# Kernel tuning notes

Measured on AMD Instinct MI355X. Metric: run time of the kernel, lower is better.

The kernel has to match this reference:

```python
import jax, jax.numpy as jnp
import numpy as np

CHUNK = 64

def depthwise_fir(x, filt):
    # x: [B,N,H,D]; filt: [H,D,K]; causal depthwise FIR conv along N
    B, N, H, D = x.shape
    K = filt.shape[-1]
    xc = x.reshape(B, N, H * D).transpose(0, 2, 1)  # [B, HD, N]
    xc = jnp.pad(xc, ((0, 0), (0, 0), (K - 1, 0)))
    w = filt.reshape(H * D, 1, K)
    y = jax.lax.conv_general_dilated(xc, w, (1,), 'VALID',
                                     feature_group_count=H * D,
                                     dimension_numbers=('NCH', 'OIH', 'NCH'))
    return y.transpose(0, 2, 1).reshape(B, N, H, D)

def delta_rule_chunkwise(q, k, v, beta, chunk=CHUNK):
    # DeltaNet chunkwise parallel delta rule. q,k,v:[B,H,L,D], beta:[B,H,L]
    B, H, L, D = q.shape
    q = q * (D ** -0.5)
    k = k / (jnp.linalg.norm(k, axis=-1, keepdims=True) + 1e-6)  # l2-norm keys (DeltaNet convention)
    v = v * beta[..., None]
    k_beta = k * beta[..., None]
    n = L // chunk
    toc = lambda t: t.reshape(B, H, n, chunk, D)
    qc, kc, vc, kbc = toc(q), toc(k), toc(v), toc(k_beta)
    # T = (I + strict_lower(k_beta k^T))^{-1} via triangular solve
    A = jnp.tril(jnp.einsum('bhncd,bhnmd->bhncm', kbc, kc), -1)
    I = jnp.eye(chunk, dtype=q.dtype)
    T = jax.scipy.linalg.solve_triangular(I + A, jnp.broadcast_to(I, A.shape), lower=True)
    u = T @ vc   # [B,H,n,c,D]
    w = T @ kbc  # [B,H,n,c,D]
    def step(S, inp):
        q_i, k_i, u_i, w_i = inp                 # [B,H,c,D]
        u_t = u_i - w_i @ S
        attn_i = jnp.tril(jnp.einsum('bhcd,bhmd->bhcm', q_i, k_i))
        o_i = q_i @ S + attn_i @ u_t
        S = S + jnp.einsum('bhcd,bhce->bhde', k_i, u_t)
        return S, o_i
    xs = tuple(jnp.moveaxis(t, 2, 0) for t in (qc, kc, u, w))
    S0 = jnp.zeros((B, H, D, D), dtype=q.dtype)
    S, o = jax.lax.scan(step, S0, xs)
    o = jnp.moveaxis(o, 0, 2).reshape(B, H, L, D)
    return o, S

def setup_inputs() -> dict:
    key = jax.random.key(0)
    B, N, C, H = 4, 1024, 768, 12
    D = C // H
    P = 5
    ks = jax.random.split(key, 16)
    s = 0.02
    fir_s = jnp.zeros((H, D, 3)).at[..., -1].set(1.0) + 0.01 * jax.random.normal(ks[1], (H, D, 3))
    fir_l = jnp.zeros((H, D, 7)).at[..., -1].set(1.0) + 0.01 * jax.random.normal(ks[2], (H, D, 7))
    return {
        'x': jax.random.normal(ks[0], (B, N, C), jnp.float32),
        'w_qkv': s * jax.random.normal(ks[3], (C, 3 * C)),
        'w_proj': s * jax.random.normal(ks[4], (C, C)),
        'b_proj': jnp.zeros((C,)),
        'fir_short_w': fir_s,
        'fir_long_w': fir_l,
        'mix': 0.02 * jax.random.normal(ks[5], (H, H)),
        'w_prune': s * jax.random.normal(ks[6], (C, H * P)),
        'b_prune': jnp.zeros((H * P,)),
        'w_g1': s * jax.random.normal(ks[7], (C, C)),
        'b_g1': jnp.zeros((C,)),
        'w_g2': s * jax.random.normal(ks[8], (C, H)),
        'b_g2': jnp.zeros((H,)),
        'w_id': s * jax.random.normal(ks[9], (C, C)),
        'id_static_logit': jnp.full((H,), float(np.log(0.2 / 0.8)), jnp.float32),
        'w_idgate': s * jax.random.normal(ks[10], (C, H)),
        'b_idgate': jnp.full((H,), -1.5, jnp.float32),
    }

def reference(x, w_qkv, w_proj, b_proj, fir_short_w, fir_long_w, mix, w_prune,
              b_prune, w_g1, b_g1, w_g2, b_g2, w_id, id_static_logit, w_idgate, b_idgate):
    B, N, C = x.shape
    H = id_static_logit.shape[0]
    D = C // H
    qkv = (x @ w_qkv).reshape(B, N, 3, H, D).transpose(2, 0, 3, 1, 4)  # [3,B,H,N,D]
    q, k, v = qkv[0], qkv[1], qkv[2]
    scale = D ** -0.5
    scores = jnp.einsum('bhqd,bhkd->bhqk', q, k) * scale
    # causal softmax attention (fp8 sage-attention math in full precision)
    neg = jnp.finfo(scores.dtype).min
    causal = jnp.tril(jnp.ones((N, N), dtype=bool))
    attn = jax.nn.softmax(jnp.where(causal, scores, neg), axis=-1)
    attn_out = jnp.einsum('bhqk,bhkd->bnhd'.replace('n', 'q'), attn, v).transpose(0, 2, 1, 3)  # [B,N,H,D] (unused downstream, kept for fidelity)
    v_reshaped = v.transpose(0, 2, 1, 3)  # [B,N,H,D]
    # identity path with static*dynamic gate
    identity_out = (x @ w_id).reshape(B, N, H, D)
    dyn_gate = jax.nn.sigmoid(x @ w_idgate + b_idgate)   # [B,N,H]
    static_gate = jax.nn.sigmoid(id_static_logit)
    identity_out = identity_out * (dyn_gate * static_gate)[..., None]
    # beta = row-sums of (non-causal) softmax, per source (== ~1 numerically)
    beta = jax.nn.softmax(scores, axis=-1).sum(-1)       # [B,H,N]
    delta_out = delta_rule_chunkwise(q, k, v, beta)[0].transpose(0, 2, 1, 3)  # [B,N,H,D]
    # FIR paths + cross-head mixing (residual head-mixing matrix)
    fir_s = depthwise_fir(v_reshaped, fir_short_w)
    fir_l = depthwise_fir(v_reshaped, fir_long_w)
    mix_s = fir_s + jnp.einsum('bnhd,hg->bngd', fir_s, mix)
    mix_l = fir_l + jnp.einsum('bnhd,hg->bngd', fir_l, mix)
    paths = jnp.stack([mix_s, mix_l, delta_out, v_reshaped, identity_out], 0)  # [P,B,N,H,D]
    P = paths.shape[0]
    # progressive pruning: per-head softmax over paths + entropy loss
    wts = jax.nn.softmax((x @ w_prune + b_prune).reshape(B, N, H, P), axis=-1)
    pruned = jnp.einsum('pbnhd,bnhp->bnhd', paths, wts)
    ent1 = -jnp.mean(jnp.sum(wts * jnp.log(wts + 1e-8), -1))
    # context gating: MLP -> per-head sigmoid gate + binary entropy loss
    hdn = jax.nn.gelu(x @ w_g1 + b_g1)
    gate = jax.nn.sigmoid(hdn @ w_g2 + b_g2)             # [B,N,H]
    context = pruned * gate[..., None]
    ent2 = -jnp.mean(gate * jnp.log(gate + 1e-8) + (1 - gate) * jnp.log(1 - gate + 1e-8))
    out = context.reshape(B, N, C) @ w_proj + b_proj
    return out, ent1 + ent2
```

## Files before the change

### kernel.cpp

```cpp
#include <hip/hip_runtime.h>
#include <hip/hip_bf16.h>
#include <math.h>

#define Bz 4
#define Nn 1024
#define Cc 768
#define Hh 12
#define Dd 64
#define BN 4096
#define NC 16
#define BH 48
#define OUT_ELEMS 3145728

#define WS_U       0u
#define WS_PLIG    3145728u
#define WS_GL      3670016u
#define WS_ENT     4194304u
#define WS_FIRST   4195328u
#define WS_FIRLT   4197632u
#define WS_CBIAS   4203008u
#define WS_GBIAS   4206976u
#define WS_SH      4207104u
#define SH_XB      0u
#define SH_QKVB    3145728u
#define SH_IDOUT   12582912u
#define SH_HDNB    15728640u
#define SH_CTXB    18874368u
#define SH_DELTA   22020096u
#define SH_QS      25165824u
#define SH_KNT     28311552u
#define SH_W       31457280u
#define SH_AT      34603008u
#define SH_WCAT2T  37748736u
#define SH_G2T     40796160u
#define SH_WPROJT  40894464u

typedef __attribute__((ext_vector_type(8))) short bf16x8;
typedef __attribute__((ext_vector_type(4))) float f32x4;

__device__ __forceinline__ float sigmoidf_(float x) { return 1.f / (1.f + __expf(-x)); }
__device__ __forceinline__ float geluf_(float x) {
    float t = tanhf(0.7978845608028654f * (x + 0.044715f * x * x * x));
    return 0.5f * x * (1.f + t);
}
__device__ __forceinline__ short bf16c(float f) {
    union { float f; unsigned u; } a; a.f = f;
    unsigned r = a.u + 0x7fffu + ((a.u >> 16) & 1u);
    return (short)(r >> 16);
}
__device__ __forceinline__ float b2f(short s) {
    union { float f; unsigned u; } a;
    a.u = ((unsigned)(unsigned short)s) << 16;
    return a.f;
}
__device__ __forceinline__ void gload16(const void* g, void* l) {
    __builtin_amdgcn_global_load_lds(
        (const __attribute__((address_space(1))) unsigned*)g,
        (__attribute__((address_space(3))) unsigned*)l, 16, 0, 0);
}
__device__ __forceinline__ bf16x8 frag_(const short* arr, int row, int kc, int quad) {
    return *(const bf16x8*)&arr[row * 64 + (((kc * 4 + quad) ^ (row & 7)) << 3)];
}

__global__ __launch_bounds__(256) void convert_x_kernel(const float* __restrict__ src,
        short* __restrict__ dst, int n4) {
    int i = blockIdx.x * 256 + threadIdx.x;
    if (i < n4) {
        float4 v = *(const float4*)&src[(size_t)i * 4];
        short4 o;
        o.x = bf16c(v.x); o.y = bf16c(v.y); o.z = bf16c(v.z); o.w = bf16c(v.w);
        *(short4*)&dst[(size_t)i * 4] = o;
    }
}

__global__ __launch_bounds__(256) void convert_w_kernel(const float* __restrict__ w_qkv,
        const float* __restrict__ w_id, const float* __restrict__ w_g1,
        const float* __restrict__ w_proj, short* __restrict__ wcat2T,
        short* __restrict__ wprojT,
        const float* __restrict__ wp, const float* __restrict__ wig,
        const float* __restrict__ bp, const float* __restrict__ big,
        const float* __restrict__ bg1, const float* __restrict__ bg2,
        const float* __restrict__ wg2, const float* __restrict__ firs,
        const float* __restrict__ firl, short* __restrict__ g2T,
        float* __restrict__ cbias, float* __restrict__ gbias,
        float* __restrict__ firsT, float* __restrict__ firlT) {
    __shared__ float t[64][65];
    const int z = blockIdx.z;
    const int tid = threadIdx.x;
    if (z == 4) {
        int i = (blockIdx.y * 12 + blockIdx.x) * 256 + tid;
        if (i < 98304) {
            int r = i / 768, k = i % 768;
            float wv = 0.f;
            if (r < 60) wv = wp[k * 60 + r];
            else if (r < 72) wv = wig[k * 12 + (r - 60)];
            wcat2T[(size_t)(3840 + r) * 768 + k] = (r < 72) ? bf16c(wv) : (short)0;
            g2T[(size_t)r * 768 + k] = (r < 12) ? bf16c(wg2[k * 12 + r]) : (short)0;
        }
        if (i < 3968) {
            float bv = 0.f;
            if (i >= 3072 && i < 3840) bv = bg1[i - 3072];
            else if (i >= 3840 && i < 3900) bv = bp[i - 3840];
            else if (i >= 3900 && i < 3912) bv = big[i - 3900];
            cbias[i] = bv;
        }
        if (i < 128) gbias[i] = (i < 12) ? bg2[i] : 0.f;
        if (i < 2304) { int tt = i / 768, e = i % 768; firsT[tt * 768 + e] = firs[e * 3 + tt]; }
        if (i < 5376) { int tt = i / 768, e = i % 768; firlT[tt * 768 + e] = firl[e * 7 + tt]; }
        return;
    }
    const float* src; short* dst; int Nw;
    if (z == 0)      { src = w_qkv;  dst = wcat2T;               Nw = 2304; }
    else if (z == 1) { src = w_id;   dst = wcat2T + 2304 * 768;  Nw = 768; }
    else if (z == 2) { src = w_g1;   dst = wcat2T + 3072 * 768;  Nw = 768; }
    else             { src = w_proj; dst = wprojT;               Nw = 768; }
    const int n0 = blockIdx.y * 64;
    if (n0 >= Nw) return;
    const int k0 = blockIdx.x * 64;
    for (int e = tid; e < 1024; e += 256) {
        int r = e >> 4, c4 = (e & 15) * 4;
        float4 v = *(const float4*)&src[(size_t)(k0 + r) * Nw + n0 + c4];
        t[c4 + 0][r] = v.x; t[c4 + 1][r] = v.y;
        t[c4 + 2][r] = v.z; t[c4 + 3][r] = v.w;
    }
    __syncthreads();
    for (int e = tid; e < 1024; e += 256) {
        int r = e >> 4, c4 = (e & 15) * 4;
        short4 o;
        o.x = bf16c(t[r][c4 + 0]); o.y = bf16c(t[r][c4 + 1]);
        o.z = bf16c(t[r][c4 + 2]); o.w = bf16c(t[r][c4 + 3]);
        *(short4*)&dst[(size_t)(n0 + r) * 768 + k0 + c4] = o;
    }
}

#define GEMM_CORE(APTR, BPTR, KDIM)                                            \
    __shared__ short As[128 * 64];                                             \
    __shared__ short Bs[128 * 64];                                             \
    const int tid = threadIdx.x;                                               \
    const int lane = tid & 63, w = tid >> 6;                                   \
    const int quad = lane >> 4, l15 = lane & 15;                               \
    const int L_ = blockIdx.y * gridDim.x + blockIdx.x;                        \
    const int xcd_ = L_ & 7, j_ = L_ >> 3;                                     \
    const int row0 = (xcd_ * 4 + (j_ & 3)) * 128, col0 = (j_ >> 2) * 128;      \
    const int wm = (w >> 1) * 64, wn = (w & 1) * 64;                           \
    int srow[4]; int scol[4];                                                  \
    _Pragma("unroll") for (int i = 0; i < 4; ++i) {                            \
        int G = (w * 4 + i) * 64 + lane;                                       \
        int row = G >> 3, g = G & 7;                                           \
        srow[i] = row;                                                         \
        scol[i] = (g ^ (row & 7)) * 8;                                         \
    }                                                                          \
    int aoff[4][2], boff[4][2];                                                \
    _Pragma("unroll") for (int mi = 0; mi < 4; ++mi)                           \
        _Pragma("unroll") for (int kk = 0; kk < 2; ++kk) {                     \
            int ra = wm + mi * 16 + l15;                                       \
            aoff[mi][kk] = ra * 128 + (((kk * 4 + quad) ^ (ra & 7)) * 16);     \
            int rb = wn + mi * 16 + l15;                                       \
            boff[mi][kk] = rb * 128 + (((kk * 4 + quad) ^ (rb & 7)) * 16);     \
        }                                                                      \
    f32x4 acc[4][4];                                                           \
    _Pragma("unroll") for (int mi = 0; mi < 4; ++mi)                           \
        _Pragma("unroll") for (int ni = 0; ni < 4; ++ni) acc[mi][ni] = (f32x4)0.f; \
    for (int k0 = 0; k0 < (KDIM); k0 += 64) {                                  \
        _Pragma("unroll") for (int i = 0; i < 4; ++i) {                        \
            gload16(&(APTR)[(size_t)(row0 + srow[i]) * (KDIM) + k0 + scol[i]], \
                    &As[(w * 4 + i) * 512]);                                   \
            gload16(&(BPTR)[(size_t)(col0 + srow[i]) * (KDIM) + k0 + scol[i]], \
                    &Bs[(w * 4 + i) * 512]);                                   \
        }                                                                      \
        __syncthreads();                                                       \
        _Pragma("unroll") for (int kk = 0; kk < 2; ++kk) {                     \
            bf16x8 af[4], bfr[4];                                              \
            _Pragma("unroll") for (int mi = 0; mi < 4; ++mi)                   \
                af[mi] = *(const bf16x8*)((const char*)As + aoff[mi][kk]);     \
            _Pragma("unroll") for (int ni = 0; ni < 4; ++ni)                   \
                bfr[ni] = *(const bf16x8*)((const char*)Bs + boff[ni][kk]);    \
            _Pragma("unroll") for (int mi = 0; mi < 4; ++mi)                   \
                _Pragma("unroll") for (int ni = 0; ni < 4; ++ni)               \
                    acc[mi][ni] = __builtin_amdgcn_mfma_f32_16x16x32_bf16(     \
                        af[mi], bfr[ni], acc[mi][ni], 0, 0, 0);                \
        }                                                                      \
        __syncthreads();                                                       \
    }

__global__ __launch_bounds__(256) void gemm_main(const short* __restrict__ A,
        const short* __restrict__ BT, const float* __restrict__ bias,
        short* __restrict__ qkvb, short* __restrict__ idoutb,
        short* __restrict__ hdnb, float* __restrict__ plig) {
    GEMM_CORE(A, BT, 768)
#pragma unroll
    for (int ni = 0; ni < 4; ++ni) {
        int col = col0 + wn + ni * 16 + l15;
        float bv = bias[col];
#pragma unroll
        for (int mi = 0; mi < 4; ++mi) {
#pragma unroll
            for (int r = 0; r < 4; ++r) {
                int row = row0 + wm + mi * 16 + quad * 4 + r;
                float v = acc[mi][ni][r] + bv;
                if (col < 2304) {
                    qkvb[(size_t)row * 2304 + col] = bf16c(v);
                } else if (col < 3072) {
                    idoutb[(size_t)row * 768 + (col - 2304)] = bf16c(v);
                } else if (col < 3840) {
                    hdnb[(size_t)row * 768 + (col - 3072)] = bf16c(geluf_(v));
                } else {
                    plig[(size_t)row * 128 + (col - 3840)] = v;
                }
            }
        }
    }
}

__global__ __launch_bounds__(256) void gemm_mfma(const short* __restrict__ A,
        const short* __restrict__ BT, const float* __restrict__ bias,
        float* __restrict__ C, int M, int N, int K) {
    GEMM_CORE(A, BT, K)
#pragma unroll
    for (int ni = 0; ni < 4; ++ni) {
        int col = col0 + wn + ni * 16 + l15;
        float bv = bias ? bias[col] : 0.f;
#pragma unroll
        for (int mi = 0; mi < 4; ++mi) {
#pragma unroll
            for (int r = 0; r < 4; ++r) {
                int row = row0 + wm + mi * 16 + quad * 4 + r;
                C[(size_t)row * N + col] = acc[mi][ni][r] + bv;
            }
        }
    }
}

__global__ __launch_bounds__(256) void pre_kernel(const short* __restrict__ qkvb,
        short* __restrict__ Qsb16, short* __restrict__ Kntb16, float* __restrict__ U,
        short* __restrict__ Wb16, short* __restrict__ Atb16) {
    __shared__ __align__(16) char smem[50176];
    float (*ts)[68] = (float (*)[68])smem;
    short* kn  = (short*)(smem + 17408);
    short* knt = (short*)(smem + 25600);
    short* qsb = (short*)(smem + 33792);
    short* vtb = (short*)(smem + 41984);
    float (*zbuf)[68] = (float (*)[68])(smem + 17408);
    short* tb  = (short*)(smem + 33792);
    const int blk = blockIdx.x;
    const int c = blk & 15, bh = blk >> 4;
    const int b = bh / Hh, h = bh % Hh;
    const int tid = threadIdx.x;
    const int lane = tid & 63, w = tid >> 6;
    const int quad = lane >> 4, l15 = lane & 15;
    const int r = tid >> 2, d0 = (tid & 3) * 16;
    const size_t rowb = ((size_t)(b * Nn + c * 64)) * 2304 + h * 64;
    const size_t base2 = (size_t)blk * 4096;

    {
        const short* qp = &qkvb[rowb + (size_t)r * 2304 + d0];
        bf16x8 qb0 = *(const bf16x8*)&qp[0],    qb1 = *(const bf16x8*)&qp[8];
        bf16x8 kb0 = *(const bf16x8*)&qp[768],  kb1 = *(const bf16x8*)&qp[776];
        bf16x8 vb0 = *(const bf16x8*)&qp[1536], vb1 = *(const bf16x8*)&qp[1544];

        float kf[16];
#pragma unroll
        for (int t = 0; t < 8; ++t) { kf[t] = b2f(kb0[t]); kf[8 + t] = b2f(kb1[t]); }
        float ss = 0.f;
#pragma unroll
        for (int t = 0; t < 16; ++t) ss += kf[t] * kf[t];
        ss += __shfl_xor(ss, 1);
        ss += __shfl_xor(ss, 2);
        float invn = 1.f / (sqrtf(ss) + 1e-6f);
        {
            bf16x8 g0, g1;
#pragma unroll
            for (int t = 0; t < 8; ++t) {
                g0[t] = bf16c(kf[t] * invn); g1[t] = bf16c(kf[8 + t] * invn);
            }
            int gb = d0 >> 3;
            *(bf16x8*)&kn[r * 64 + (((gb + 0) ^ (r & 7)) << 3)] = g0;
            *(bf16x8*)&kn[r * 64 + (((gb + 1) ^ (r & 7)) << 3)] = g1;
#pragma unroll
            for (int t = 0; t < 8; ++t) {
                int d = d0 + t;
                knt[d * 64 + (((r >> 3) ^ (d & 7)) << 3) + (r & 7)] = g0[t];
                int d2 = d0 + 8 + t;
                knt[d2 * 64 + (((r >> 3) ^ (d2 & 7)) << 3) + (r & 7)] = g1[t];
            }
        }
        {
            bf16x8 g0, g1;
#pragma unroll
            for (int t = 0; t < 8; ++t) {
                g0[t] = bf16c(b2f(qb0[t]) * 0.125f);
                g1[t] = bf16c(b2f(qb1[t]) * 0.125f);
            }
            int gb = d0 >> 3;
            *(bf16x8*)&qsb[r * 64 + (((gb + 0) ^ (r & 7)) << 3)] = g0;
            *(bf16x8*)&qsb[r * 64 + (((gb + 1) ^ (r & 7)) << 3)] = g1;
            *(bf16x8*)&Qsb16[base2 + r * 64 + d0] = g0;
            *(bf16x8*)&Qsb16[base2 + r * 64 + d0 + 8] = g1;
        }
#pragma unroll
        for (int t = 0; t < 8; ++t) {
            int d = d0 + t;
            vtb[d * 64 + (((r >> 3) ^ (d & 7)) << 3) + (r & 7)] = vb0[t];
            int d2 = d0 + 8 + t;
            vtb[d2 * 64 + (((r >> 3) ^ (d2 & 7)) << 3) + (r & 7)] = vb1[t];
        }
    }
    __syncthreads();

    f32x4 accT[4];
    {
        const int ar = w * 16 + l15;
        bf16x8 aK0 = frag_(kn, ar, 0, quad), aK1 = frag_(kn, ar, 1, quad);
        bf16x8 aQ0 = frag_(qsb, ar, 0, quad), aQ1 = frag_(qsb, ar, 1, quad);
        f32x4 accA[4];
#pragma unroll
        for (int ni = 0; ni < 4; ++ni) {
            int br = ni * 16 + l15;
            bf16x8 b0 = frag_(kn, br, 0, quad), b1 = frag_(kn, br, 1, quad);
            accA[ni] = __builtin_amdgcn_mfma_f32_16x16x32_bf16(aK0, b0, (f32x4)0.f, 0, 0, 0);
            accA[ni] = __builtin_amdgcn_mfma_f32_16x16x32_bf16(aK1, b1, accA[ni], 0, 0, 0);
            accT[ni] = __builtin_amdgcn_mfma_f32_16x16x32_bf16(aQ0, b0, (f32x4)0.f, 0, 0, 0);
            accT[ni] = __builtin_amdgcn_mfma_f32_16x16x32_bf16(aQ1, b1, accT[ni], 0, 0, 0);
        }
#pragma unroll
        for (int ni = 0; ni < 4; ++ni)
#pragma unroll
            for (int reg = 0; reg < 4; ++reg) {
                int row = w * 16 + quad * 4 + reg;
                int col = ni * 16 + l15;
                ts[row][col] = (col < row) ? accA[ni][reg] : 0.f;
            }
    }
    __syncthreads();

    {
        const int R0 = w * 16;
        const int j = lane & 15, s = lane >> 4;
#pragma unroll 1
        for (int i = 0; i < 16; ++i) {
            float p = 0.f;
            for (int m = s; m < i; m += 4)
                p += ts[R0 + i][R0 + m] * ts[R0 + m][R0 + j];
            p += __shfl_xor(p, 16);
            p += __shfl_xor(p, 32);
            if (s == 0) ts[R0 + i][R0 + j] = ((j == i) ? 1.f : 0.f) - p;
        }
    }
    __syncthreads();
#pragma unroll 1
    for (int I = 1; I < 4; ++I) {
        const int ncol = I * 16;
        for (int e = tid; e < 16 * ncol; e += 256) {
            int i = e / ncol, jj = e % ncol;
            float s = 0.f;
            for (int m = jj; m < ncol; ++m) s += ts[ncol + i][m] * ts[m][jj];
            zbuf[i][jj] = s;
        }
        __syncthreads();
        for (int e = tid; e < 16 * ncol; e += 256) {
            int i = e / ncol, jj = e % ncol;
            float s = 0.f;
            for (int ml = 0; ml <= i; ++ml) s += ts[ncol + i][ncol + ml] * zbuf[ml][jj];
            ts[ncol + i][jj] = -s;
        }
        __syncthreads();
    }
    for (int e = tid; e < 512; e += 256) {
        int row = e >> 3, g = e & 7;
        bf16x8 o;
#pragma unroll
        for (int t = 0; t < 8; ++t) o[t] = bf16c(ts[row][g * 8 + t]);
        *(bf16x8*)&tb[row * 64 + ((g ^ (row & 7)) << 3)] = o;
    }
    __syncthreads();

    f32x4 accW[4], accU[4];
    {
        const int ar = w * 16 + l15;
        bf16x8 aT0 = frag_(tb, ar, 0, quad), aT1 = frag_(tb, ar, 1, quad);
#pragma unroll
        for (int ni = 0; ni < 4; ++ni) {
            int br = ni * 16 + l15;
            bf16x8 b0 = frag_(knt, br, 0, quad), b1 = frag_(knt, br, 1, quad);
            bf16x8 c0 = frag_(vtb, br, 0, quad), c1 = frag_(vtb, br, 1, quad);
            accW[ni] = __builtin_amdgcn_mfma_f32_16x16x32_bf16(aT0, b0, (f32x4)0.f, 0, 0, 0);
            accW[ni] = __builtin_amdgcn_mfma_f32_16x16x32_bf16(aT1, b1, accW[ni], 0, 0, 0);
            accU[ni] = __builtin_amdgcn_mfma_f32_16x16x32_bf16(aT0, c0, (f32x4)0.f, 0, 0, 0);
            accU[ni] = __builtin_amdgcn_mfma_f32_16x16x32_bf16(aT1, c1, accU[ni], 0, 0, 0);
        }
    }
#pragma unroll
    for (int ni = 0; ni < 4; ++ni)
#pragma unroll
        for (int reg = 0; reg < 4; ++reg) {
            int row = w * 16 + quad * 4 + reg;
            int col = ni * 16 + l15;
            Wb16[base2 + (size_t)row * 64 + col] = bf16c(accW[ni][reg]);
            U[base2 + (size_t)row * 64 + col] = accU[ni][reg];
            Atb16[base2 + (size_t)row * 64 + col] =
                (col <= row) ? bf16c(accT[ni][reg]) : (short)0;
        }
    for (int e = tid; e < 512; e += 256) {
        int row = e >> 3, gl = e & 7;
        *(bf16x8*)&Kntb16[base2 + row * 64 + ((gl ^ (row & 7)) << 3)] =
            *(const bf16x8*)&knt[row * 64 + (gl << 3)];
    }
}

#define LOADF(cc, F, UU) {                                                     \
    size_t tb_ = ((size_t)(bh * 16 + (cc))) * 4096;                            \
    F##0 = *(const bf16x8*)&Wb16[tb_ + off0];                                  \
    F##1 = *(const bf16x8*)&Wb16[tb_ + off1];                                  \
    F##2 = *(const bf16x8*)&Qsb16[tb_ + off0];                                 \
    F##3 = *(const bf16x8*)&Qsb16[tb_ + off1];                                 \
    F##4 = *(const bf16x8*)&Atb16[tb_ + off0];                                 \
    F##5 = *(const bf16x8*)&Atb16[tb_ + off1];                                 \
    F##6 = *(const bf16x8*)&Kntb16[tb_ + off0];                                \
    F##7 = *(const bf16x8*)&Kntb16[tb_ + off1];                                \
    UU##0 = U[tb_ + urow + 0 * 64]; UU##1 = U[tb_ + urow + 1 * 64];            \
    UU##2 = U[tb_ + urow + 2 * 64]; UU##3 = U[tb_ + urow + 3 * 64]; }

#define BODY(c, F, UU, FN, UN) {                                               \
    int cn_ = ((c) + 1 < 16) ? (c) + 1 : 0;                                    \
    LOADF(cn_, FN, UN);                                                        \
    bf16x8 st0 = *(const bf16x8*)&ST[stoff0];                                  \
    bf16x8 st1 = *(const bf16x8*)&ST[stoff1];                                  \
    bf16x8 nw0, nw1;                                                           \
    _Pragma("unroll") for (int t_ = 0; t_ < 8; ++t_) {                         \
        nw0[t_] = F##0[t_] ^ (short)0x8000;                                    \
        nw1[t_] = F##1[t_] ^ (short)0x8000; }                                  \
    f32x4 ut = {UU##0, UU##1, UU##2, UU##3};                                   \
    ut = __builtin_amdgcn_mfma_f32_16x16x32_bf16(nw0, st0, ut, 0, 0, 0);       \
    ut = __builtin_amdgcn_mfma_f32_16x16x32_bf16(nw1, st1, ut, 0, 0, 0);       \
    f32x4 o = (f32x4)0.f;                                                      \
    o = __builtin_amdgcn_mfma_f32_16x16x32_bf16(F##2, st0, o, 0, 0, 0);        \
    o = __builtin_amdgcn_mfma_f32_16x16x32_bf16(F##3, st1, o, 0, 0, 0);        \
    _Pragma("unroll") for (int j_ = 0; j_ < 4; ++j_) {                         \
        int rr_ = R0 + quad * 4 + j_;                                          \
        UT[l15 * 64 + (((rr_ >> 3) ^ (l15 & 7)) << 3) + (rr_ & 7)] = bf16c(ut[j_]); } \
    __syncthreads();                                                           \
    bf16x8 uf0 = *(const bf16x8*)&UT[stoff0];                                  \
    bf16x8 uf1 = *(const bf16x8*)&UT[stoff1];                                  \
    o = __builtin_amdgcn_mfma_f32_16x16x32_bf16(F##4, uf0, o, 0, 0, 0);        \
    o = __builtin_amdgcn_mfma_f32_16x16x32_bf16(F##5, uf1, o, 0, 0, 0);        \
    S = __builtin_amdgcn_mfma_f32_16x16x32_bf16(F##6, uf0, S, 0, 0, 0);        \
    S = __builtin_amdgcn_mfma_f32_16x16x32_bf16(F##7, uf1, S, 0, 0, 0);        \
    _Pragma("unroll") for (int j_ = 0; j_ < 4; ++j_)                           \
        deltab[obase + (size_t)((c) * 64 + j_) * 768] = bf16c(o[j_]);          \
    _Pragma("unroll") for (int j_ = 0; j_ < 4; ++j_) {                         \
        int dd_ = R0 + quad * 4 + j_;                                          \
        ST[l15 * 64 + (((dd_ >> 3) ^ (l15 & 7)) << 3) + (dd_ & 7)] = bf16c(S[j_]); } \
    __syncthreads(); }

__global__ __launch_bounds__(256) void scan_kernel(const short* __restrict__ Qsb16,
        const short* __restrict__ Kntb16, const float* __restrict__ U,
        const short* __restrict__ Wb16, const short* __restrict__ Atb16,
        short* __restrict__ deltab) {
    __shared__ short ST[1024];
    __shared__ short UT[1024];
    const int bh = blockIdx.x;
    const int b = bh / Hh, h = bh % Hh;
    const int g0 = blockIdx.y * 16;
    const int tid = threadIdx.x;
    const int lane = tid & 63, w = tid >> 6;
    const int quad = lane >> 4, l15 = lane & 15;
    const int R0 = w * 16;
    const int off0 = (R0 + l15) * 64 + quad * 8;
    const int off1 = off0 + 32;
    const int urow = (R0 + quad * 4) * 64 + g0 + l15;
    const int stoff0 = l15 * 64 + ((quad ^ (l15 & 7)) << 3);
    const int stoff1 = l15 * 64 + (((4 + quad) ^ (l15 & 7)) << 3);
    const size_t obase = ((size_t)(b * Nn + R0 + quad * 4)) * 768 + h * 64 + g0 + l15;

    for (int e = tid; e < 512; e += 256) ((int*)ST)[e] = 0;
    f32x4 S = (f32x4)0.f;
    bf16x8 fA0, fA1, fA2, fA3, fA4, fA5, fA6, fA7;
    bf16x8 fB0, fB1, fB2, fB3, fB4, fB5, fB6, fB7;
    float uA0, uA1, uA2, uA3, uB0, uB1, uB2, uB3;
    LOADF(0, fA, uA);
    __syncthreads();
#pragma unroll 1
    for (int c = 0; c < 16; c += 2) {
        BODY(c, fA, uA, fB, uB);
        BODY(c + 1, fB, uB, fA, uA);
    }
}

__global__ __launch_bounds__(256) void paths_kernel(const short* __restrict__ qkvb,
        const short* __restrict__ deltab, const short* __restrict__ idoutb,
        const float* __restrict__ plig, const float* __restrict__ gl,
        const float* __restrict__ mixw, const float* __restrict__ idst,
        const float* __restrict__ firsT, const float* __restrict__ firlT,
        short* __restrict__ ctxb, float* __restrict__ entslots) {
    __shared__ float vt[10][768];
    __shared__ float fsb[768], flb[768];
    __shared__ float wts4[4][60], gate4[4][12], idg4[4][12];
    __shared__ float entb[48];
    const int blk = blockIdx.x;
    const int b = blk >> 8, n0 = (blk & 255) * 4;
    const int tid = threadIdx.x;

    for (int t = tid; t < 960; t += 256) {
        int row = t / 96, c8 = (t % 96) * 8;
        int np = n0 - 6 + row;
        float4 lo = make_float4(0.f, 0.f, 0.f, 0.f);
        float4 hi = make_float4(0.f, 0.f, 0.f, 0.f);
        if (np >= 0) {
            bf16x8 vv = *(const bf16x8*)&qkvb[((size_t)((b << 10) + np)) * 2304 + 1536 + c8];
            lo.x = b2f(vv[0]); lo.y = b2f(vv[1]); lo.z = b2f(vv[2]); lo.w = b2f(vv[3]);
            hi.x = b2f(vv[4]); hi.y = b2f(vv[5]); hi.z = b2f(vv[6]); hi.w = b2f(vv[7]);
        }
        *(float4*)&vt[row][c8] = lo;
        *(float4*)&vt[row][c8 + 4] = hi;
    }
    if (tid < 48) {
        int ni = tid / 12, h = tid % 12;
        int bn = (b << 10) + n0 + ni;
        const float* pb = &plig[(size_t)bn * 128];
        float lg[5]; float mx = -1e30f;
#pragma unroll
        for (int p = 0; p < 5; ++p) { lg[p] = pb[h * 5 + p]; mx = fmaxf(mx, lg[p]); }
        float sum = 0.f;
#pragma unroll
        for (int p = 0; p < 5; ++p) { lg[p] = __expf(lg[p] - mx); sum += lg[p]; }
        float e1 = 0.f;
#pragma unroll
        for (int p = 0; p < 5; ++p) {
            float wv = lg[p] / sum;
            wts4[ni][h * 5 + p] = wv;
            e1 += wv * logf(wv + 1e-8f);
        }
        float g = sigmoidf_(gl[(size_t)bn * 128 + h]);
        gate4[ni][h] = g;
        float e2 = g * logf(g + 1e-8f) + (1.f - g) * logf(1.f - g + 1e-8f);
        idg4[ni][h] = sigmoidf_(pb[60 + h]) * sigmoidf_(idst[h]);
        entb[tid] = e1 + e2;
    }
    float4 wl[7], wsv[3];
    if (tid < 192) {
        int c4 = tid * 4;
#pragma unroll
        for (int t = 0; t < 7; ++t) wl[t] = *(const float4*)&firlT[t * 768 + c4];
#pragma unroll
        for (int t = 0; t < 3; ++t) wsv[t] = *(const float4*)&firsT[t * 768 + c4];
    }
    __syncthreads();

#pragma unroll 1
    for (int ni = 0; ni < 4; ++ni) {
        if (tid < 192) {
            int c4 = tid * 4;
            float4 as = make_float4(0.f, 0.f, 0.f, 0.f);
            float4 al = make_float4(0.f, 0.f, 0.f, 0.f);
#pragma unroll
            for (int t = 0; t < 7; ++t) {
                float4 vv = *(const float4*)&vt[ni + t][c4];
                al.x += wl[t].x * vv.x; al.y += wl[t].y * vv.y;
                al.z += wl[t].z * vv.z; al.w += wl[t].w * vv.w;
                if (t >= 4) {
                    as.x += wsv[t - 4].x * vv.x; as.y += wsv[t - 4].y * vv.y;
                    as.z += wsv[t - 4].z * vv.z; as.w += wsv[t - 4].w * vv.w;
                }
            }
            *(float4*)&fsb[c4] = as;
            *(float4*)&flb[c4] = al;
        }
        __syncthreads();
        if (tid < 192) {
            int c4 = tid * 4;
            int h = c4 >> 6, d = c4 & 63;
            float4 ms = *(const float4*)&fsb[c4];
            float4 ml = *(const float4*)&flb[c4];
#pragma unroll
            for (int hh = 0; hh < 12; ++hh) {
                float mw = mixw[hh * 12 + h];
                float4 fsv = *(const float4*)&fsb[hh * 64 + d];
                float4 flv = *(const float4*)&flb[hh * 64 + d];
                ms.x += mw * fsv.x; ms.y += mw * fsv.y;
                ms.z += mw * fsv.z; ms.w += mw * fsv.w;
                ml.x += mw * flv.x; ml.y += mw * flv.y;
                ml.z += mw * flv.z; ml.w += mw * flv.w;
            }
            int bn = (b << 10) + n0 + ni;
            short4 ds = *(const short4*)&deltab[(size_t)bn * 768 + c4];
            short4 is = *(const short4*)&idoutb[(size_t)bn * 768 + c4];
            float4 vv = *(const float4*)&vt[ni + 6][c4];
            float ig = idg4[ni][h];
            const float* wp = &wts4[ni][h * 5];
            float4 pr;
            pr.x = ms.x * wp[0] + ml.x * wp[1] + b2f(ds.x) * wp[2] + vv.x * wp[3] + b2f(is.x) * ig * wp[4];
            pr.y = ms.y * wp[0] + ml.y * wp[1] + b2f(ds.y) * wp[2] + vv.y * wp[3] + b2f(is.y) * ig * wp[4];
            pr.z = ms.z * wp[0] + ml.z * wp[1] + b2f(ds.z) * wp[2] + vv.z * wp[3] + b2f(is.z) * ig * wp[4];
            pr.w = ms.w * wp[0] + ml.w * wp[1] + b2f(ds.w) * wp[2] + vv.w * wp[3] + b2f(is.w) * ig * wp[4];
            float g = gate4[ni][h];
            short4 o;
            o.x = bf16c(pr.x * g); o.y = bf16c(pr.y * g);
            o.z = bf16c(pr.z * g); o.w = bf16c(pr.w * g);
            *(short4*)&ctxb[(size_t)bn * 768 + c4] = o;
        }
        __syncthreads();
    }
    if (tid == 0) {
        float s = 0.f;
#pragma unroll
        for (int i = 0; i < 48; ++i) s += entb[i];
        entslots[blk] = s;
    }
}

__global__ __launch_bounds__(256) void finalize_kernel(const float* __restrict__ slots,
        float* __restrict__ out) {
    __shared__ float red[256];
    const int tid = threadIdx.x;
    float s = 0.f;
    for (int i = tid; i < 1024; i += 256) s += slots[i];
    red[tid] = s;
    __syncthreads();
    for (int off = 128; off > 0; off >>= 1) {
        if (tid < off) red[tid] += red[tid + off];
        __syncthreads();
    }
    if (tid == 0) out[OUT_ELEMS] = -red[0] * (1.f / 49152.f);
}

extern "C" void kernel_launch(void* const* d_in, const int* in_sizes, int n_in,
                              void* d_out, int out_size, void* d_ws, size_t ws_size,
                              hipStream_t stream) {
    const float* x        = (const float*)d_in[0];
    const float* w_qkv    = (const float*)d_in[1];
    const float* w_proj   = (const float*)d_in[2];
    const float* b_proj   = (const float*)d_in[3];
    const float* fir_s_w  = (const float*)d_in[4];
    const float* fir_l_w  = (const float*)d_in[5];
    const float* mixw     = (const float*)d_in[6];
    const float* w_prune  = (const float*)d_in[7];
    const float* b_prune  = (const float*)d_in[8];
    const float* w_g1     = (const float*)d_in[9];
    const float* b_g1     = (const float*)d_in[10];
    const float* w_g2     = (const float*)d_in[11];
    const float* b_g2     = (const float*)d_in[12];
    const float* w_id     = (const float*)d_in[13];
    const float* id_st    = (const float*)d_in[14];
    const float* w_idgate = (const float*)d_in[15];
    const float* b_idgate = (const float*)d_in[16];
    float* out = (float*)d_out;
    float* ws  = (float*)d_ws;

    float* Ub    = ws + WS_U;
    float* plig  = ws + WS_PLIG;
    float* gl    = ws + WS_GL;
    float* ent   = ws + WS_ENT;
    float* firsT = ws + WS_FIRST;
    float* firlT = ws + WS_FIRLT;
    float* cbias = ws + WS_CBIAS;
    float* gbias = ws + WS_GBIAS;
    short* wsh   = (short*)(ws + WS_SH);
    short* xb      = wsh + SH_XB;
    short* qkvb    = wsh + SH_QKVB;
    short* idoutb  = wsh + SH_IDOUT;
    short* hdnb    = wsh + SH_HDNB;
    short* ctxb    = wsh + SH_CTXB;
    short* deltab  = wsh + SH_DELTA;
    short* Qsb16   = wsh + SH_QS;
    short* Kntb16  = wsh + SH_KNT;
    short* Wb16    = wsh + SH_W;
    short* Atb16   = wsh + SH_AT;
    short* wcat2T  = wsh + SH_WCAT2T;
    short* g2T     = wsh + SH_G2T;
    short* wprojT  = wsh + SH_WPROJT;

    convert_x_kernel<<<dim3(3072), 256, 0, stream>>>(x, xb, 786432);
    convert_w_kernel<<<dim3(12, 36, 5), 256, 0, stream>>>(w_qkv, w_id, w_g1, w_proj,
            wcat2T, wprojT, w_prune, w_idgate, b_prune, b_idgate, b_g1, b_g2,
            w_g2, fir_s_w, fir_l_w, g2T, cbias, gbias, firsT, firlT);
    gemm_main<<<dim3(31, 32), 256, 0, stream>>>(xb, wcat2T, cbias,
                                                qkvb, idoutb, hdnb, plig);
    gemm_mfma<<<dim3(1, 32), 256, 0, stream>>>(hdnb, g2T, gbias, gl, BN, 128, 768);
    pre_kernel<<<dim3(BH * NC), 256, 0, stream>>>(qkvb, Qsb16, Kntb16, Ub, Wb16, Atb16);
    scan_kernel<<<dim3(BH, 4), 256, 0, stream>>>(Qsb16, Kntb16, Ub, Wb16, Atb16, deltab);
    paths_kernel<<<dim3(1024), 256, 0, stream>>>(qkvb, deltab, idoutb, plig, gl,
                                                 mixw, id_st, firsT, firlT, ctxb, ent);
    gemm_mfma<<<dim3(6, 32), 256, 0, stream>>>(ctxb, wprojT, b_proj, out, BN, 768, 768);
    finalize_kernel<<<1, 256, 0, stream>>>(ent, out);
}
```

Before: 258.2 us.

## Merge small kernels to cut launch count: fold x-convert, gate GEMM, finalize

Folds the x fp32->bf16 conversion into the weight-conversion kernel as an extra z-slice, runs the small gate GEMM (hdn @ w_g2) as 32 extra blocks inside the delta-rule preprocessing kernel, and moves the entropy finalize reduction into the last projection GEMM. This drops three kernel launches and the serialization gaps between them. In exchange, one GEMM block does the serial reduction, and the gate GEMM blocks share a launch with the heavier preprocessing blocks, which can unbalance that launch.

```diff
diff --git a/kernel.cpp b/kernel.cpp
--- a/kernel.cpp
+++ b/kernel.cpp
@@ -62,17 +62,6 @@
     return *(const bf16x8*)&arr[row * 64 + (((kc * 4 + quad) ^ (row & 7)) << 3)];
 }
 
-__global__ __launch_bounds__(256) void convert_x_kernel(const float* __restrict__ src,
-        short* __restrict__ dst, int n4) {
-    int i = blockIdx.x * 256 + threadIdx.x;
-    if (i < n4) {
-        float4 v = *(const float4*)&src[(size_t)i * 4];
-        short4 o;
-        o.x = bf16c(v.x); o.y = bf16c(v.y); o.z = bf16c(v.z); o.w = bf16c(v.w);
-        *(short4*)&dst[(size_t)i * 4] = o;
-    }
-}
-
 __global__ __launch_bounds__(256) void convert_w_kernel(const float* __restrict__ w_qkv,
         const float* __restrict__ w_id, const float* __restrict__ w_g1,
         const float* __restrict__ w_proj, short* __restrict__ wcat2T,
@@ -83,10 +72,21 @@
         const float* __restrict__ wg2, const float* __restrict__ firs,
         const float* __restrict__ firl, short* __restrict__ g2T,
         float* __restrict__ cbias, float* __restrict__ gbias,
-        float* __restrict__ firsT, float* __restrict__ firlT) {
+        float* __restrict__ firsT, float* __restrict__ firlT,
+        const float* __restrict__ x, short* __restrict__ xb) {
     __shared__ float t[64][65];
     const int z = blockIdx.z;
     const int tid = threadIdx.x;
+    if (z == 5) {
+        for (int i = (blockIdx.y * 12 + blockIdx.x) * 256 + tid; i < 786432;
+             i += 110592) {
+            float4 v = *(const float4*)&x[(size_t)i * 4];
+            short4 o;
+            o.x = bf16c(v.x); o.y = bf16c(v.y); o.z = bf16c(v.z); o.w = bf16c(v.w);
+            *(short4*)&xb[(size_t)i * 4] = o;
+        }
+        return;
+    }
     if (z == 4) {
         int i = (blockIdx.y * 12 + blockIdx.x) * 256 + tid;
         if (i < 98304) {
@@ -214,7 +214,9 @@
 
 __global__ __launch_bounds__(256) void gemm_mfma(const short* __restrict__ A,
         const short* __restrict__ BT, const float* __restrict__ bias,
-        float* __restrict__ C, int M, int N, int K) {
+        float* __restrict__ C, int M, int N, int K,
+        const float* __restrict__ slots, float* __restrict__ entout) {
+    __shared__ float red[256];
     GEMM_CORE(A, BT, K)
 #pragma unroll
     for (int ni = 0; ni < 4; ++ni) {
@@ -229,12 +231,100 @@
             }
         }
     }
-}
-
-__global__ __launch_bounds__(256) void pre_kernel(const short* __restrict__ qkvb,
+    if (slots && L_ == 0) {
+        float s = 0.f;
+        for (int i = tid; i < 1024; i += 256) s += slots[i];
+        red[tid] = s;
+        __syncthreads();
+        for (int off = 128; off > 0; off >>= 1) {
+            if (tid < off) red[tid] += red[tid + off];
+            __syncthreads();
+        }
+        if (tid == 0) entout[0] = -red[0] * (1.f / 49152.f);
+    }
+}
+
+__global__ __launch_bounds__(256) void pre_gl_kernel(const short* __restrict__ qkvb,
         short* __restrict__ Qsb16, short* __restrict__ Kntb16, float* __restrict__ U,
-        short* __restrict__ Wb16, short* __restrict__ Atb16) {
+        short* __restrict__ Wb16, short* __restrict__ Atb16,
+        const short* __restrict__ hdnb, const short* __restrict__ g2T,
+        const float* __restrict__ gbias, float* __restrict__ gl) {
     __shared__ __align__(16) char smem[50176];
+    const int blk = blockIdx.x;
+    const int tid = threadIdx.x;
+    const int lane = tid & 63, w = tid >> 6;
+    const int quad = lane >> 4, l15 = lane & 15;
+
+    if (blk >= 768) {
+        short* As = (short*)smem;
+        short* Bs = (short*)(smem + 16384);
+        const int row0 = (blk - 768) * 128;
+        const int wm = (w >> 1) * 64, wn = (w & 1) * 64;
+        int srow[4], scol[4];
+#pragma unroll
+        for (int i = 0; i < 4; ++i) {
+            int G = (w * 4 + i) * 64 + lane;
+            int row = G >> 3, g = G & 7;
+            srow[i] = row;
+            scol[i] = (g ^ (row & 7)) * 8;
+        }
+        int aoff[4][2], boff[4][2];
+#pragma unroll
+        for (int mi = 0; mi < 4; ++mi)
+#pragma unroll
+            for (int kk = 0; kk < 2; ++kk) {
+                int ra = wm + mi * 16 + l15;
+                aoff[mi][kk] = ra * 128 + (((kk * 4 + quad) ^ (ra & 7)) * 16);
+                int rb = wn + mi * 16 + l15;
+                boff[mi][kk] = rb * 128 + (((kk * 4 + quad) ^ (rb & 7)) * 16);
+            }
+        f32x4 acc[4][4];
+#pragma unroll
+        for (int mi = 0; mi < 4; ++mi)
+#pragma unroll
+            for (int ni = 0; ni < 4; ++ni) acc[mi][ni] = (f32x4)0.f;
+        for (int k0 = 0; k0 < 768; k0 += 64) {
+#pragma unroll
+            for (int i = 0; i < 4; ++i) {
+                gload16(&hdnb[(size_t)(row0 + srow[i]) * 768 + k0 + scol[i]],
+                        &As[(w * 4 + i) * 512]);
+                gload16(&g2T[(size_t)srow[i] * 768 + k0 + scol[i]],
+                        &Bs[(w * 4 + i) * 512]);
+            }
+            __syncthreads();
+#pragma unroll
+            for (int kk = 0; kk < 2; ++kk) {
+                bf16x8 af[4], bfr[4];
+#pragma unroll
+                for (int mi = 0; mi < 4; ++mi)
+                    af[mi] = *(const bf16x8*)((const char*)As + aoff[mi][kk]);
+#pragma unroll
+                for (int ni = 0; ni < 4; ++ni)
+                    bfr[ni] = *(const bf16x8*)((const char*)Bs + boff[ni][kk]);
+#pragma unroll
+                for (int mi = 0; mi < 4; ++mi)
+#pragma unroll
+                    for (int ni = 0; ni < 4; ++ni)
+                        acc[mi][ni] = __builtin_amdgcn_mfma_f32_16x16x32_bf16(
+                            af[mi], bfr[ni], acc[mi][ni], 0, 0, 0);
+            }
+            __syncthreads();
+        }
+#pragma unroll
+        for (int ni = 0; ni < 4; ++ni) {
+            int col = wn + ni * 16 + l15;
+            float bv = gbias[col];
+#pragma unroll
+            for (int mi = 0; mi < 4; ++mi)
+#pragma unroll
+                for (int r = 0; r < 4; ++r) {
+                    int row = row0 + wm + mi * 16 + quad * 4 + r;
+                    gl[(size_t)row * 128 + col] = acc[mi][ni][r] + bv;
+                }
+        }
+        return;
+    }
+
     float (*ts)[68] = (float (*)[68])smem;
     short* kn  = (short*)(smem + 17408);
     short* knt = (short*)(smem + 25600);
@@ -242,12 +332,8 @@
     short* vtb = (short*)(smem + 41984);
     float (*zbuf)[68] = (float (*)[68])(smem + 17408);
     short* tb  = (short*)(smem + 33792);
-    const int blk = blockIdx.x;
     const int c = blk & 15, bh = blk >> 4;
     const int b = bh / Hh, h = bh % Hh;
-    const int tid = threadIdx.x;
-    const int lane = tid & 63, w = tid >> 6;
-    const int quad = lane >> 4, l15 = lane & 15;
     const int r = tid >> 2, d0 = (tid & 3) * 16;
     const size_t rowb = ((size_t)(b * Nn + c * 64)) * 2304 + h * 64;
     const size_t base2 = (size_t)blk * 4096;
@@ -401,9 +487,9 @@
                 (col <= row) ? bf16c(accT[ni][reg]) : (short)0;
         }
     for (int e = tid; e < 512; e += 256) {
-        int row = e >> 3, gl = e & 7;
-        *(bf16x8*)&Kntb16[base2 + row * 64 + ((gl ^ (row & 7)) << 3)] =
-            *(const bf16x8*)&knt[row * 64 + (gl << 3)];
+        int row = e >> 3, gl2 = e & 7;
+        *(bf16x8*)&Kntb16[base2 + row * 64 + ((gl2 ^ (row & 7)) << 3)] =
+            *(const bf16x8*)&knt[row * 64 + (gl2 << 3)];
     }
 }
 
@@ -608,21 +694,6 @@
     }
 }
 
-__global__ __launch_bounds__(256) void finalize_kernel(const float* __restrict__ slots,
-        float* __restrict__ out) {
-    __shared__ float red[256];
-    const int tid = threadIdx.x;
-    float s = 0.f;
-    for (int i = tid; i < 1024; i += 256) s += slots[i];
-    red[tid] = s;
-    __syncthreads();
-    for (int off = 128; off > 0; off >>= 1) {
-        if (tid < off) red[tid] += red[tid + off];
-        __syncthreads();
-    }
-    if (tid == 0) out[OUT_ELEMS] = -red[0] * (1.f / 49152.f);
-}
-
 extern "C" void kernel_launch(void* const* d_in, const int* in_sizes, int n_in,
                               void* d_out, int out_size, void* d_ws, size_t ws_size,
                               hipStream_t stream) {
@@ -669,17 +740,16 @@
     short* g2T     = wsh + SH_G2T;
     short* wprojT  = wsh + SH_WPROJT;
 
-    convert_x_kernel<<<dim3(3072), 256, 0, stream>>>(x, xb, 786432);
-    convert_w_kernel<<<dim3(12, 36, 5), 256, 0, stream>>>(w_qkv, w_id, w_g1, w_proj,
+    convert_w_kernel<<<dim3(12, 36, 6), 256, 0, stream>>>(w_qkv, w_id, w_g1, w_proj,
             wcat2T, wprojT, w_prune, w_idgate, b_prune, b_idgate, b_g1, b_g2,
-            w_g2, fir_s_w, fir_l_w, g2T, cbias, gbias, firsT, firlT);
+            w_g2, fir_s_w, fir_l_w, g2T, cbias, gbias, firsT, firlT, x, xb);
     gemm_main<<<dim3(31, 32), 256, 0, stream>>>(xb, wcat2T, cbias,
                                                 qkvb, idoutb, hdnb, plig);
-    gemm_mfma<<<dim3(1, 32), 256, 0, stream>>>(hdnb, g2T, gbias, gl, BN, 128, 768);
-    pre_kernel<<<dim3(BH * NC), 256, 0, stream>>>(qkvb, Qsb16, Kntb16, Ub, Wb16, Atb16);
+    pre_gl_kernel<<<dim3(800), 256, 0, stream>>>(qkvb, Qsb16, Kntb16, Ub, Wb16, Atb16,
+                                                 hdnb, g2T, gbias, gl);
     scan_kernel<<<dim3(BH, 4), 256, 0, stream>>>(Qsb16, Kntb16, Ub, Wb16, Atb16, deltab);
     paths_kernel<<<dim3(1024), 256, 0, stream>>>(qkvb, deltab, idoutb, plig, gl,
                                                  mixw, id_st, firsT, firlT, ctxb, ent);
-    gemm_mfma<<<dim3(6, 32), 256, 0, stream>>>(ctxb, wprojT, b_proj, out, BN, 768, 768);
-    finalize_kernel<<<1, 256, 0, stream>>>(ent, out);
-}
+    gemm_mfma<<<dim3(6, 32), 256, 0, stream>>>(ctxb, wprojT, b_proj, out, BN, 768, 768,
+                                               ent, out + OUT_ELEMS);
+}
```

Result: slower. 263.5 us (+2.1%).
